# Performance work log

Hardware: AMD Instinct MI355X
Metric: run time of the kernel (lower is better)

Reference implementation:

```python
import jax, jax.numpy as jnp
import numpy as np


def setup_inputs() -> dict:
    key = jax.random.key(0)
    features = jax.random.normal(key, (8192, 512), dtype=jnp.float32)
    return {"features": features}


def reference(features):
    # Pairwise L2 distance via the GEMM trick (avoids the N x N x D broadcast
    # intermediate the original torch code materializes):
    #   ||a - b||^2 = ||a||^2 + ||b||^2 - 2 a.b
    sq_norms = jnp.sum(features * features, axis=-1)            # [N]
    gram = features @ features.T                                # [N, N]
    sq_dist = sq_norms[:, None] + sq_norms[None, :] - 2.0 * gram
    sq_dist = jnp.maximum(sq_dist, 0.0)                         # clamp fp noise
    return -jnp.sqrt(sq_dist)                                   # [N, N]
```

## Files before the change

kernel.cpp:

```cpp
#include <hip/hip_runtime.h>
#include <math.h>

#define N_ROWS 8192
#define DIM    512
#define NT     (N_ROWS / 128)
#define NBLK   (NT * (NT + 1) / 2)

typedef __bf16 bf16x8 __attribute__((ext_vector_type(8)));
typedef float  floatx4 __attribute__((ext_vector_type(4)));

__device__ __forceinline__ unsigned short f2bf_rne(float x) {
    union { float f; unsigned u; } v; v.f = x;
    unsigned r = v.u + 0x7FFFu + ((v.u >> 16) & 1u);
    return (unsigned short)(r >> 16);
}

__device__ __forceinline__ void async_cp16(const void* g, void* l) {
    __builtin_amdgcn_global_load_lds(
        (const __attribute__((address_space(1))) unsigned int*)g,
        (__attribute__((address_space(3))) unsigned int*)l,
        16, 0, 0);
}

__global__ __launch_bounds__(256) void fs_norm_convert(
    const float* __restrict__ F, unsigned short* __restrict__ Fb,
    float* __restrict__ sn) {
    const int wave = threadIdx.x >> 6;
    const int lane = threadIdx.x & 63;
    const int row  = blockIdx.x * 4 + wave;

    const float4* src = reinterpret_cast<const float4*>(F + (size_t)row * DIM) + lane * 2;
    float4 x0 = src[0];
    float4 x1 = src[1];

    float ss = x0.x*x0.x + x0.y*x0.y + x0.z*x0.z + x0.w*x0.w
             + x1.x*x1.x + x1.y*x1.y + x1.z*x1.z + x1.w*x1.w;

    uint4 p;
    p.x = (unsigned)f2bf_rne(x0.x) | ((unsigned)f2bf_rne(x0.y) << 16);
    p.y = (unsigned)f2bf_rne(x0.z) | ((unsigned)f2bf_rne(x0.w) << 16);
    p.z = (unsigned)f2bf_rne(x1.x) | ((unsigned)f2bf_rne(x1.y) << 16);
    p.w = (unsigned)f2bf_rne(x1.z) | ((unsigned)f2bf_rne(x1.w) << 16);
    reinterpret_cast<uint4*>(Fb + (size_t)row * DIM)[lane] = p;

    #pragma unroll
    for (int off = 32; off > 0; off >>= 1) ss += __shfl_down(ss, off);
    if (lane == 0) sn[row] = ss;
}

__global__ __launch_bounds__(256, 2) void fs_gemm_sym(
    const unsigned short* __restrict__ Fb, const float* __restrict__ sn,
    float* __restrict__ out) {
    __shared__ unsigned short smem[4][128 * 64];

    const int tid  = threadIdx.x;
    const int lane = tid & 63;
    const int wave = tid >> 6;
    const int wr   = wave >> 1;
    const int wc   = wave & 1;
    const int quad = lane >> 4;
    const int l16  = lane & 15;

    int L = (int)blockIdx.x;
    L = (L & 7) * (NBLK / 8) + (L >> 3);
    int bi = (int)((sqrtf(8.0f * (float)L + 1.0f) - 1.0f) * 0.5f);
    while ((bi + 1) * (bi + 2) / 2 <= L) ++bi;
    while (bi * (bi + 1) / 2 > L) --bi;
    const int bj   = L - bi * (bi + 1) / 2;
    const int diag = (bi == bj);

    const int bRow = bi * 128;
    const int bCol = bj * 128;

    floatx4 acc[4][4];
    #pragma unroll
    for (int i = 0; i < 4; ++i)
        #pragma unroll
        for (int j = 0; j < 4; ++j)
            acc[i][j] = floatx4{0.f, 0.f, 0.f, 0.f};

    const int r   = tid >> 3;
    const int c   = tid & 7;
    const int csw = c ^ (r & 7);
    const unsigned short* gA = Fb + (size_t)(bRow + r) * DIM + csw * 8;
    const unsigned short* gB = Fb + (size_t)(bCol + r) * DIM + csw * 8;

    const int cg0 = ((0 + quad) ^ (l16 & 7)) * 8;
    const int cg1 = ((4 + quad) ^ (l16 & 7)) * 8;

    #define STAGE(buf, k0) {                                        \
        unsigned short* la = &smem[buf][tid * 8];                   \
        unsigned short* lb = &smem[2 + (buf)][tid * 8];             \
        const unsigned short* pa = gA + (k0);                       \
        const unsigned short* pb = gB + (k0);                       \
        async_cp16(pa,            la);                              \
        async_cp16(pa + 32 * DIM, la + 2048);                       \
        async_cp16(pa + 64 * DIM, la + 4096);                       \
        async_cp16(pa + 96 * DIM, la + 6144);                       \
        async_cp16(pb,            lb);                              \
        async_cp16(pb + 32 * DIM, lb + 2048);                       \
        async_cp16(pb + 64 * DIM, lb + 4096);                       \
        async_cp16(pb + 96 * DIM, lb + 6144);                       \
    }

    STAGE(0, 0)
    __syncthreads();

    for (int k = 0; k < DIM / 64; ++k) {
        if (k < DIM / 64 - 1) STAGE((k + 1) & 1, (k + 1) * 64)
        const unsigned short* Ab = smem[k & 1];
        const unsigned short* Bb = smem[2 + (k & 1)];
        #pragma unroll
        for (int h = 0; h < 2; ++h) {
            const int cg = h ? cg1 : cg0;
            bf16x8 af[4], bf[4];
            #pragma unroll
            for (int t = 0; t < 4; ++t) {
                af[t] = *reinterpret_cast<const bf16x8*>(
                    Ab + (wr * 64 + t * 16 + l16) * 64 + cg);
                bf[t] = *reinterpret_cast<const bf16x8*>(
                    Bb + (wc * 64 + t * 16 + l16) * 64 + cg);
            }
            #pragma unroll
            for (int i = 0; i < 4; ++i)
                #pragma unroll
                for (int j = 0; j < 4; ++j)
                    acc[i][j] = __builtin_amdgcn_mfma_f32_16x16x32_bf16(
                        af[i], bf[j], acc[i][j], 0, 0, 0);
        }
        __syncthreads();
    }
    float* tbuf = reinterpret_cast<float*>(&smem[0][0]) + wave * 4096;

    const int row0 = bRow + wr * 64;
    const int col0 = bCol + wc * 64;
    {
        float snc[4];
        #pragma unroll
        for (int j = 0; j < 4; ++j) snc[j] = sn[col0 + j * 16 + l16];

        #pragma unroll
        for (int i = 0; i < 4; ++i) {
            #pragma unroll
            for (int rr = 0; rr < 4; ++rr) {
                const int rloc = i * 16 + quad * 4 + rr;
                const int row  = row0 + rloc;
                const float snr = sn[row];
                float* orow = out + (size_t)row * N_ROWS;
                #pragma unroll
                for (int j = 0; j < 4; ++j) {
                    const int cloc = j * 16 + l16;
                    const int col  = col0 + cloc;
                    float v = snr + snc[j] - 2.0f * acc[i][j][rr];
                    float o = (row == col) ? 0.0f : -sqrtf(fmaxf(v, 0.0f));
                    orow[col] = o;
                    tbuf[cloc * 64 + (rloc ^ (cloc & 31))] = o;
                }
            }
        }
    }

    if (!diag) {
        #pragma unroll
        for (int p = 0; p < 4; ++p) {
            #pragma unroll
            for (int rr = 0; rr < 4; ++rr) {
                const int rT  = p * 16 + quad * 4 + rr;
                const int row = bCol + wc * 64 + rT;
                float* orow = out + (size_t)row * N_ROWS;
                #pragma unroll
                for (int q = 0; q < 4; ++q) {
                    const int cT = q * 16 + l16;
                    orow[bRow + wr * 64 + cT] =
                        tbuf[rT * 64 + (cT ^ (rT & 31))];
                }
            }
        }
    }
}

extern "C" void kernel_launch(void* const* d_in, const int* in_sizes, int n_in,
                              void* d_out, int out_size, void* d_ws, size_t ws_size,
                              hipStream_t stream) {
    const float* F = (const float*)d_in[0];
    float* out = (float*)d_out;

    unsigned short* Fb = (unsigned short*)d_ws;
    float* sn = (float*)((char*)d_ws + (size_t)N_ROWS * DIM * 2);

    fs_norm_convert<<<N_ROWS / 4, 256, 0, stream>>>(F, Fb, sn);

    fs_gemm_sym<<<dim3(NBLK), 256, 0, stream>>>(Fb, sn, out);
}
```

Measured before the change: 326.6 us.

## Write mirrored tile directly with vector nontemporal stores, drop LDS transpose

The epilogue no longer stages the tile in LDS to write its transposed mirror. Each lane already holds four consecutive rows for one column in the MFMA accumulator layout, so it writes that float4 straight to the transposed location. All output stores become nontemporal, row norms are loaded as a vector, and the final barrier is dropped. This removes the LDS round-trip and a set of scalar stores. The risk is that the primary-direction stores stay scalar and strided, and skipping the last barrier is only safe because LDS is no longer reused.

```diff
diff --git a/kernel.cpp b/kernel.cpp
--- a/kernel.cpp
+++ b/kernel.cpp
@@ -51,7 +51,8 @@
 __global__ __launch_bounds__(256, 2) void fs_gemm_sym(
     const unsigned short* __restrict__ Fb, const float* __restrict__ sn,
     float* __restrict__ out) {
-    __shared__ unsigned short smem[4][128 * 64];
+    __shared__ unsigned short As[2][128 * 64];
+    __shared__ unsigned short Bs[2][128 * 64];
 
     const int tid  = threadIdx.x;
     const int lane = tid & 63;
@@ -89,8 +90,8 @@
     const int cg1 = ((4 + quad) ^ (l16 & 7)) * 8;
 
     #define STAGE(buf, k0) {                                        \
-        unsigned short* la = &smem[buf][tid * 8];                   \
-        unsigned short* lb = &smem[2 + (buf)][tid * 8];             \
+        unsigned short* la = &As[buf][tid * 8];                     \
+        unsigned short* lb = &Bs[buf][tid * 8];                     \
         const unsigned short* pa = gA + (k0);                       \
         const unsigned short* pb = gB + (k0);                       \
         async_cp16(pa,            la);                              \
@@ -108,8 +109,8 @@
 
     for (int k = 0; k < DIM / 64; ++k) {
         if (k < DIM / 64 - 1) STAGE((k + 1) & 1, (k + 1) * 64)
-        const unsigned short* Ab = smem[k & 1];
-        const unsigned short* Bb = smem[2 + (k & 1)];
+        const unsigned short* Ab = As[k & 1];
+        const unsigned short* Bb = Bs[k & 1];
         #pragma unroll
         for (int h = 0; h < 2; ++h) {
             const int cg = h ? cg1 : cg0;
@@ -128,53 +129,37 @@
                     acc[i][j] = __builtin_amdgcn_mfma_f32_16x16x32_bf16(
                         af[i], bf[j], acc[i][j], 0, 0, 0);
         }
-        __syncthreads();
+        if (k < DIM / 64 - 1) __syncthreads();
     }
-    float* tbuf = reinterpret_cast<float*>(&smem[0][0]) + wave * 4096;
 
     const int row0 = bRow + wr * 64;
     const int col0 = bCol + wc * 64;
-    {
-        float snc[4];
+    float snc[4];
+    #pragma unroll
+    for (int j = 0; j < 4; ++j) snc[j] = sn[col0 + j * 16 + l16];
+
+    #pragma unroll
+    for (int i = 0; i < 4; ++i) {
+        const int rbase = row0 + i * 16 + quad * 4;
+        const floatx4 snr4 = *reinterpret_cast<const floatx4*>(sn + rbase);
         #pragma unroll
-        for (int j = 0; j < 4; ++j) snc[j] = sn[col0 + j * 16 + l16];
-
-        #pragma unroll
-        for (int i = 0; i < 4; ++i) {
+        for (int j = 0; j < 4; ++j) {
+            const int col = col0 + j * 16 + l16;
+            floatx4 ov;
             #pragma unroll
             for (int rr = 0; rr < 4; ++rr) {
-                const int rloc = i * 16 + quad * 4 + rr;
-                const int row  = row0 + rloc;
-                const float snr = sn[row];
-                float* orow = out + (size_t)row * N_ROWS;
-                #pragma unroll
-                for (int j = 0; j < 4; ++j) {
-                    const int cloc = j * 16 + l16;
-                    const int col  = col0 + cloc;
-                    float v = snr + snc[j] - 2.0f * acc[i][j][rr];
-                    float o = (row == col) ? 0.0f : -sqrtf(fmaxf(v, 0.0f));
-                    orow[col] = o;
-                    tbuf[cloc * 64 + (rloc ^ (cloc & 31))] = o;
-                }
+                float v = snr4[rr] + snc[j] - 2.0f * acc[i][j][rr];
+                float o = -sqrtf(fmaxf(v, 0.0f));
+                ov[rr] = (rbase + rr == col) ? 0.0f : o;
             }
-        }
-    }
-
-    if (!diag) {
-        #pragma unroll
-        for (int p = 0; p < 4; ++p) {
             #pragma unroll
-            for (int rr = 0; rr < 4; ++rr) {
-                const int rT  = p * 16 + quad * 4 + rr;
-                const int row = bCol + wc * 64 + rT;
-                float* orow = out + (size_t)row * N_ROWS;
-                #pragma unroll
-                for (int q = 0; q < 4; ++q) {
-                    const int cT = q * 16 + l16;
-                    orow[bRow + wr * 64 + cT] =
-                        tbuf[rT * 64 + (cT ^ (rT & 31))];
-                }
-            }
+            for (int rr = 0; rr < 4; ++rr)
+                __builtin_nontemporal_store(
+                    ov[rr], out + (size_t)(rbase + rr) * N_ROWS + col);
+            if (!diag)
+                __builtin_nontemporal_store(
+                    ov, reinterpret_cast<floatx4*>(
+                            out + (size_t)col * N_ROWS + rbase));
         }
     }
 }
```

Measured after the change: 330.5 us. About the same (+1.2%).
